# Kernel optimization log

Measured on AMD Instinct MI355X. Metric: run time of the kernel, lower is better.

## Reference

```python
import jax, jax.numpy as jnp
import numpy as np

B, N, C, H = 2, 2048, 1024, 16
D = C // H  # head_dim = 64


def setup_inputs() -> dict:
    key = jax.random.key(0)
    k1, k2, k3, k4 = jax.random.split(key, 4)
    x = jax.random.normal(k1, (B, N, C), dtype=jnp.float32)
    # params (torch Linear: y = x @ W.T + b). Store as [in, out] for einsum.
    w_qkv = jax.random.normal(k2, (C, 3 * C), dtype=jnp.float32) * (1.0 / np.sqrt(C))
    w_out = jax.random.normal(k3, (C, C), dtype=jnp.float32) * (1.0 / np.sqrt(C))
    b_out = jax.random.normal(k4, (C,), dtype=jnp.float32) * 0.01
    # causal mask: 1 above the diagonal -> masked_fill(-inf)
    attn_mask = jnp.triu(jnp.ones((N, N), dtype=jnp.int32), k=1)
    return {"x": x, "w_qkv": w_qkv, "w_out": w_out, "b_out": b_out, "attn_mask": attn_mask}


def reference(x, w_qkv, w_out, b_out, attn_mask):
    b, n, c = x.shape
    scale = 1.0 / jnp.sqrt(jnp.asarray(D, dtype=x.dtype))
    qkv = jnp.einsum('bnc,cd->bnd', x, w_qkv)                # [B, N, 3C]
    qkv = qkv.reshape(b, n, 3, H, D)
    q = qkv[:, :, 0].transpose(0, 2, 1, 3)                   # [B, H, N, D]
    k = qkv[:, :, 1].transpose(0, 2, 1, 3)
    v = qkv[:, :, 2].transpose(0, 2, 1, 3)
    scores = jnp.einsum('bhqd,bhkd->bhqk', q, k) * scale     # [B, H, N, N]
    scores = jnp.where(attn_mask == 1, jnp.asarray(-jnp.inf, dtype=scores.dtype), scores)
    attn = jax.nn.softmax(scores, axis=-1)
    # dropout is identity in eval mode (deterministic reference)
    out = jnp.einsum('bhqk,bhkd->bhqd', attn, v)             # [B, H, N, D]
    out = out.transpose(0, 2, 1, 3).reshape(b, n, c)         # [B, N, C]
    return jnp.einsum('bnc,cd->bnd', out, w_out) + b_out
```

## Files before the change

kernel.cpp:

```cpp
#include <hip/hip_runtime.h>

typedef _Float16 f16;
typedef _Float16 f16x8 __attribute__((ext_vector_type(8)));
typedef _Float16 f16x4 __attribute__((ext_vector_type(4)));
typedef float    f32x4 __attribute__((ext_vector_type(4)));

#define MFMA16(a, b, c) __builtin_amdgcn_mfma_f32_16x16x32_f16((a), (b), (c), 0, 0, 0)

__device__ __forceinline__ void gload16(const void* g, void* l) {
  __builtin_amdgcn_global_load_lds(
      (const __attribute__((address_space(1))) unsigned int*)g,
      (__attribute__((address_space(3))) unsigned int*)l, 16, 0, 0);
}

__device__ __forceinline__ float ex2(float x) {
  float r;
  asm("v_exp_f32 %0, %1" : "=v"(r) : "v"(x));
  return r;
}

#define WAITV(N) asm volatile("s_waitcnt vmcnt(" #N ")" ::: "memory")
#define BARRIER() __builtin_amdgcn_s_barrier()
#define CFENCE() asm volatile("" ::: "memory")

__global__ void prep(const float* __restrict__ x, f16* __restrict__ xh,
                     const float* __restrict__ wqkv, f16* __restrict__ oqkv,
                     const float* __restrict__ wout, f16* __restrict__ oout) {
  __shared__ float tile[32][33];
  int bx = blockIdx.x, t = threadIdx.x;
  if (bx < 4096) {
    int i = bx * 256 + t;
    float4 v = ((const float4*)x)[i];
    f16x4 o;
    o.x = (f16)v.x; o.y = (f16)v.y; o.z = (f16)v.z; o.w = (f16)v.w;
    ((f16x4*)xh)[i] = o;
    return;
  }
  int tb = bx - 4096;
  int bx2 = tb & 127, by = tb >> 7;
  const float* in;
  f16* out;
  int Cc, c0;
  if (bx2 < 96) { in = wqkv; out = oqkv; Cc = 3072; c0 = bx2 * 32; }
  else          { in = wout; out = oout; Cc = 1024; c0 = (bx2 - 96) * 32; }
  int r0 = by * 32;
  int tx = t & 31, ty = t >> 5;
#pragma unroll
  for (int i = ty; i < 32; i += 8)
    tile[i][tx] = in[(size_t)(r0 + i) * Cc + c0 + tx];
  __syncthreads();
#pragma unroll
  for (int i = ty; i < 32; i += 8)
    out[(size_t)(c0 + i) * 1024 + r0 + tx] = (f16)tile[tx][i];
}

template <int KDIM>
__device__ __forceinline__ void gemm_core(const f16* __restrict__ A, const f16* __restrict__ Bt,
                                          int bm, int bn, f16* lA, f16* lB, f32x4 acc[4][4]) {
  const int t = threadIdx.x, lane = t & 63, wave = t >> 6;
  const int wm = wave >> 1, wn = wave & 1;
  const int srow = lane >> 3;
  const int skb = (lane & 7) * 16;
  const int nkt = KDIM / 64;
  for (int kt = 0; kt < nkt; ++kt) {
    __syncthreads();
#pragma unroll
    for (int c = 0; c < 4; ++c) {
      int cc = c * 4 + wave;
      int row = cc * 8 + srow;
      int kbs = skb ^ ((row & 7) << 4);
      gload16((const char*)A + (size_t)(bm * 128 + row) * (KDIM * 2) + kt * 128 + kbs,
              lA + cc * 512);
      gload16((const char*)Bt + (size_t)(bn * 128 + row) * (KDIM * 2) + kt * 128 + kbs,
              lB + cc * 512);
    }
    __syncthreads();
#pragma unroll
    for (int ks = 0; ks < 2; ++ks) {
      f16x8 af[4], bf[4];
#pragma unroll
      for (int mi = 0; mi < 4; ++mi) {
        int r = wm * 64 + mi * 16 + (lane & 15);
        int ke = (ks * 32 + ((lane >> 4) << 3)) ^ ((r & 7) << 3);
        af[mi] = *(const f16x8*)&lA[r * 64 + ke];
      }
#pragma unroll
      for (int ni = 0; ni < 4; ++ni) {
        int r = wn * 64 + ni * 16 + (lane & 15);
        int ke = (ks * 32 + ((lane >> 4) << 3)) ^ ((r & 7) << 3);
        bf[ni] = *(const f16x8*)&lB[r * 64 + ke];
      }
#pragma unroll
      for (int mi = 0; mi < 4; ++mi)
#pragma unroll
        for (int ni = 0; ni < 4; ++ni)
          acc[mi][ni] = MFMA16(af[mi], bf[ni], acc[mi][ni]);
    }
  }
}

template <int KDIM>
__device__ __forceinline__ void gemm_core64(const f16* __restrict__ A, const f16* __restrict__ Bt,
                                            int bm, int bn, f16* lA, f16* lB, f32x4 acc[2][4]) {
  const int t = threadIdx.x, lane = t & 63, wave = t >> 6;
  const int wm = wave >> 1, wn = wave & 1;
  const int srow = lane >> 3;
  const int skb = (lane & 7) * 16;
  const int nkt = KDIM / 64;
  for (int kt = 0; kt < nkt; ++kt) {
    __syncthreads();
#pragma unroll
    for (int c = 0; c < 2; ++c) {
      int cc = c * 4 + wave;
      int row = cc * 8 + srow;
      int kbs = skb ^ ((row & 7) << 4);
      gload16((const char*)A + (size_t)(bm * 64 + row) * (KDIM * 2) + kt * 128 + kbs,
              lA + cc * 512);
    }
#pragma unroll
    for (int c = 0; c < 4; ++c) {
      int cc = c * 4 + wave;
      int row = cc * 8 + srow;
      int kbs = skb ^ ((row & 7) << 4);
      gload16((const char*)Bt + (size_t)(bn * 128 + row) * (KDIM * 2) + kt * 128 + kbs,
              lB + cc * 512);
    }
    __syncthreads();
#pragma unroll
    for (int ks = 0; ks < 2; ++ks) {
      f16x8 af[2], bf[4];
#pragma unroll
      for (int mi = 0; mi < 2; ++mi) {
        int r = wm * 32 + mi * 16 + (lane & 15);
        int ke = (ks * 32 + ((lane >> 4) << 3)) ^ ((r & 7) << 3);
        af[mi] = *(const f16x8*)&lA[r * 64 + ke];
      }
#pragma unroll
      for (int ni = 0; ni < 4; ++ni) {
        int r = wn * 64 + ni * 16 + (lane & 15);
        int ke = (ks * 32 + ((lane >> 4) << 3)) ^ ((r & 7) << 3);
        bf[ni] = *(const f16x8*)&lB[r * 64 + ke];
      }
#pragma unroll
      for (int mi = 0; mi < 2; ++mi)
#pragma unroll
        for (int ni = 0; ni < 4; ++ni)
          acc[mi][ni] = MFMA16(af[mi], bf[ni], acc[mi][ni]);
    }
  }
}

__global__ __launch_bounds__(256, 2) void gemm_qkv(const f16* __restrict__ A,
                                                   const f16* __restrict__ Bt,
                                                   f16* __restrict__ Qo, f16* __restrict__ Ko,
                                                   f16* __restrict__ Vt) {
  __shared__ __align__(16) f16 smem[128 * 136];
  f16* lA = smem;
  f16* lB = smem + 8192;
  f32x4 acc[4][4] = {};
  int w = blockIdx.x;
  int xcd = w & 7, i = w >> 3;
  int xr = xcd >> 1, xc = xcd & 1;
  int bm = xr * 8 + (i & 7);
  int bn = xc * 12 + (i >> 3);
  gemm_core<1024>(A, Bt, bm, bn, lA, lB, acc);
  int lane = threadIdx.x & 63, wave = threadIdx.x >> 6;
  int wm = wave >> 1, wn = wave & 1;
  int g = lane >> 4, q15 = lane & 15;
  int sec = (bn * 128) >> 10;
  if (sec < 2) {
    float scl = (sec == 0) ? 0.18033688f : 1.0f;
#pragma unroll
    for (int mi = 0; mi < 4; ++mi)
#pragma unroll
      for (int ni = 0; ni < 4; ++ni)
#pragma unroll
        for (int reg = 0; reg < 4; ++reg) {
          int gr = bm * 128 + wm * 64 + mi * 16 + (g << 2) + reg;
          int gc = bn * 128 + wn * 64 + ni * 16 + q15;
          int b = gr >> 11, n = gr & 2047;
          int jj = gc & 1023;
          int h = jj >> 6, d = jj & 63;
          f16 v = (f16)(acc[mi][ni][reg] * scl);
          size_t bh = (size_t)(b * 16 + h);
          if (sec == 0) Qo[(bh * 2048 + n) * 64 + d] = v;
          else          Ko[(bh * 2048 + n) * 64 + d] = v;
        }
  } else {
    __syncthreads();
#pragma unroll
    for (int mi = 0; mi < 4; ++mi)
#pragma unroll
      for (int ni = 0; ni < 4; ++ni)
#pragma unroll
        for (int reg = 0; reg < 4; ++reg) {
          int rl = wm * 64 + mi * 16 + (g << 2) + reg;
          int cl = wn * 64 + ni * 16 + q15;
          int r5 = rl & 31;
          int rlp = (rl & ~31) | (((r5 >> 2) & 3) << 3) | (((r5 >> 4) & 1) << 2) | (r5 & 3);
          smem[cl * 136 + rlp] = (f16)acc[mi][ni][reg];
        }
    __syncthreads();
    int tid = threadIdx.x;
    int cl = tid >> 1, half = tid & 1;
    int jj = (bn * 128 + cl) & 1023;
    int h = jj >> 6, d = jj & 63;
    int b = (bm * 128) >> 11;
    size_t bh = (size_t)(b * 16 + h);
    f16* dst = Vt + (bh * 64 + d) * 2048 + (bm * 128 & 2047) + half * 64;
    const f16* src = smem + cl * 136 + half * 64;
#pragma unroll
    for (int j8 = 0; j8 < 8; ++j8)
      *(f16x8*)&dst[j8 * 8] = *(const f16x8*)&src[j8 * 8];
  }
}

__device__ __forceinline__ void attn_one(const f16* __restrict__ Qb, const f16* __restrict__ Kb,
                                         const f16* __restrict__ Vb, f16* __restrict__ Ob,
                                         int qt, int lane, int wave, f16* lK, f16* lV) {
  const int N = 2048;
  const int wq0 = qt * 64 + wave * 16;
  const int g = lane >> 4, q15 = lane & 15;
  f16x8 qf[2];
#pragma unroll
  for (int ks = 0; ks < 2; ++ks)
    qf[ks] = *(const f16x8*)&Qb[(size_t)(wq0 + q15) * 64 + ks * 32 + (g << 3)];
  f32x4 oacc[4] = {};
  float mrun = -1e30f, lrun = 0.f;
  const int srow = lane >> 3, skb = (lane & 7) * 16;
  const int ntiles = qt + 1;

  auto STAGE = [&](int buf, int kv) {
    int kv0 = kv << 6;
#pragma unroll
    for (int c = 0; c < 2; ++c) {
      int cc = c * 4 + wave;
      int row = cc * 8 + srow;
      int kbs = skb ^ ((row & 7) << 4);
      gload16((const char*)Kb + (size_t)(kv0 + row) * 128 + kbs, lK + buf * 4096 + cc * 512);
      gload16((const char*)Vb + (size_t)row * (N * 2) + (size_t)kv0 * 2 + kbs,
              lV + buf * 4096 + cc * 512);
    }
  };

  STAGE(0, 0);
  if (ntiles > 1) STAGE(1, 1);
  for (int kv = 0; kv < ntiles; ++kv) {
    int cur = kv & 1;
    if (kv + 1 < ntiles) WAITV(4); else WAITV(0);
    BARRIER();
    const f16* K0 = lK + cur * 4096;
    const f16* V0 = lV + cur * 4096;
    int kv0 = kv << 6;
    f32x4 s[4] = {};
    __builtin_amdgcn_s_setprio(1);
#pragma unroll
    for (int ks = 0; ks < 2; ++ks) {
      f16x8 kf[4];
#pragma unroll
      for (int ni = 0; ni < 4; ++ni) {
        int r = ni * 16 + q15;
        int ke = (ks * 32 + (g << 3)) ^ ((r & 7) << 3);
        kf[ni] = *(const f16x8*)&K0[r * 64 + ke];
      }
#pragma unroll
      for (int ni = 0; ni < 4; ++ni) s[ni] = MFMA16(kf[ni], qf[ks], s[ni]);
    }
    __builtin_amdgcn_s_setprio(0);
    if (kv == qt) {
      int gq = wq0 + q15;
#pragma unroll
      for (int ni = 0; ni < 4; ++ni)
#pragma unroll
        for (int reg = 0; reg < 4; ++reg) {
          int gk = kv0 + ni * 16 + g * 4 + reg;
          if (gk > gq) s[ni][reg] = -1e30f;
        }
    }
    f32x4 m4 = s[0];
#pragma unroll
    for (int ni = 1; ni < 4; ++ni)
#pragma unroll
      for (int reg = 0; reg < 4; ++reg) m4[reg] = fmaxf(m4[reg], s[ni][reg]);
    float mx = fmaxf(fmaxf(m4[0], m4[1]), fmaxf(m4[2], m4[3]));
    mx = fmaxf(mx, __shfl_xor(mx, 16));
    mx = fmaxf(mx, __shfl_xor(mx, 32));
    if (__any(mx > mrun)) {
      float mnew = fmaxf(mrun, mx);
      float corr = ex2(mrun - mnew);
      mrun = mnew;
      lrun *= corr;
#pragma unroll
      for (int ni = 0; ni < 4; ++ni)
#pragma unroll
        for (int reg = 0; reg < 4; ++reg) oacc[ni][reg] *= corr;
    }
#pragma unroll
    for (int ni = 0; ni < 4; ++ni)
#pragma unroll
      for (int reg = 0; reg < 4; ++reg) s[ni][reg] = ex2(s[ni][reg] - mrun);
    f32x4 racc = (s[0] + s[1]) + (s[2] + s[3]);
    float rsum = (racc[0] + racc[1]) + (racc[2] + racc[3]);
    rsum += __shfl_xor(rsum, 16);
    rsum += __shfl_xor(rsum, 32);
    lrun += rsum;
    f16x8 pf[2];
#pragma unroll
    for (int ks = 0; ks < 2; ++ks)
#pragma unroll
      for (int e = 0; e < 8; ++e) pf[ks][e] = (f16)s[2 * ks + (e >> 2)][e & 3];
    __builtin_amdgcn_s_setprio(1);
#pragma unroll
    for (int ks = 0; ks < 2; ++ks) {
      f16x8 vf[4];
#pragma unroll
      for (int mi = 0; mi < 4; ++mi) {
        int r = mi * 16 + q15;
        int ke = (ks * 32 + (g << 3)) ^ ((r & 7) << 3);
        vf[mi] = *(const f16x8*)&V0[r * 64 + ke];
      }
#pragma unroll
      for (int mi = 0; mi < 4; ++mi) oacc[mi] = MFMA16(vf[mi], pf[ks], oacc[mi]);
    }
    __builtin_amdgcn_s_setprio(0);
    BARRIER();
    CFENCE();
    if (kv + 2 < ntiles) STAGE(cur, kv + 2);
  }
  float inv = 1.0f / lrun;
  int gq = wq0 + q15;
#pragma unroll
  for (int mi = 0; mi < 4; ++mi) {
    f16x4 o4;
#pragma unroll
    for (int reg = 0; reg < 4; ++reg) o4[reg] = (f16)(oacc[mi][reg] * inv);
    *(f16x4*)&Ob[(size_t)gq * 1024 + mi * 16 + g * 4] = o4;
  }
}

__global__ __launch_bounds__(256, 4) void attn(const f16* __restrict__ Q,
                                               const f16* __restrict__ K,
                                               const f16* __restrict__ Vt,
                                               f16* __restrict__ O) {
  __shared__ __align__(16) f16 lK[2 * 4096];
  __shared__ __align__(16) f16 lV[2 * 4096];
  int w = blockIdx.x;
  int c = w & 7, j = w >> 3;
  int a = j >> 5, k = j & 31;
  int bh = c * 4 + a;
  int kk = (a >= 2) ? ((k + 8) & 31) : k;
  int qt = (a & 1) ? (31 - kk) : kk;
  int b = bh >> 4, h = bh & 15;
  int lane = threadIdx.x & 63, wave = threadIdx.x >> 6;
  const f16* Qb = Q + (size_t)bh * 2048 * 64;
  const f16* Kb = K + (size_t)bh * 2048 * 64;
  const f16* Vb = Vt + (size_t)bh * 2048 * 64;
  f16* Ob = O + (size_t)b * 2048 * 1024 + h * 64;
  attn_one(Qb, Kb, Vb, Ob, qt, lane, wave, lK, lV);
}

__global__ __launch_bounds__(256, 2) void gemm_out(const f16* __restrict__ A,
                                                   const f16* __restrict__ Bt,
                                                   const float* __restrict__ bias,
                                                   float* __restrict__ out) {
  __shared__ __align__(16) f16 smem[12288];
  f16* lA = smem;
  f16* lB = smem + 4096;
  f32x4 acc[2][4] = {};
  int w = blockIdx.x;
  int xcd = w & 7, i = w >> 3;
  int bm = xcd * 8 + (i & 7);
  int bn = i >> 3;
  gemm_core64<1024>(A, Bt, bm, bn, lA, lB, acc);
  int lane = threadIdx.x & 63, wave = threadIdx.x >> 6;
  int wm = wave >> 1, wn = wave & 1;
#pragma unroll
  for (int mi = 0; mi < 2; ++mi)
#pragma unroll
    for (int ni = 0; ni < 4; ++ni)
#pragma unroll
      for (int reg = 0; reg < 4; ++reg) {
        int gr = bm * 64 + wm * 32 + mi * 16 + ((lane >> 4) << 2) + reg;
        int gc = bn * 128 + wn * 64 + ni * 16 + (lane & 15);
        out[(size_t)gr * 1024 + gc] = acc[mi][ni][reg] + bias[gc];
      }
}

extern "C" void kernel_launch(void* const* d_in, const int* in_sizes, int n_in,
                              void* d_out, int out_size, void* d_ws, size_t ws_size,
                              hipStream_t stream) {
  const float* x     = (const float*)d_in[0];
  const float* w_qkv = (const float*)d_in[1];
  const float* w_out = (const float*)d_in[2];
  const float* b_out = (const float*)d_in[3];
  float* out = (float*)d_out;
  char* ws = (char*)d_ws;

  f16* xh    = (f16*)(ws);
  f16* wqkvT = (f16*)(ws + (8u << 20));
  f16* woutT = (f16*)(ws + (14u << 20));
  f16* Qs    = (f16*)(ws + (16u << 20));
  f16* Ks    = (f16*)(ws + (24u << 20));
  f16* Vts   = (f16*)(ws + (32u << 20));
  f16* Oa    = (f16*)(ws + (40u << 20));

  prep<<<4096 + 128 * 32, 256, 0, stream>>>(x, xh, w_qkv, wqkvT, w_out, woutT);
  gemm_qkv<<<768, 256, 0, stream>>>(xh, wqkvT, Qs, Ks, Vts);
  attn<<<1024, 256, 0, stream>>>(Qs, Ks, Vts, Oa);
  gemm_out<<<512, 256, 0, stream>>>(Oa, woutT, b_out, out);
}
```

Baseline: 100.8 us.

## Split attention KV range across two wave pairs with 32-row KV tiles and merge

Restructures the attention kernel so the block's four waves form two pairs. Each pair processes half of the causal KV range in 32-key tiles, and each wave handles 32 query rows instead of 16. At the end, pair 1 writes its partial output, running max and running sum to LDS, and pair 0 merges them with a rescaling step. The intent is to halve the serial KV loop length per block and reuse each K/V fragment across two query subtiles, at the cost of a final merge step, extra LDS traffic and more registers.

```diff
diff --git a/kernel.cpp b/kernel.cpp
--- a/kernel.cpp
+++ b/kernel.cpp
@@ -215,135 +215,11 @@
   }
 }
 
-__device__ __forceinline__ void attn_one(const f16* __restrict__ Qb, const f16* __restrict__ Kb,
-                                         const f16* __restrict__ Vb, f16* __restrict__ Ob,
-                                         int qt, int lane, int wave, f16* lK, f16* lV) {
-  const int N = 2048;
-  const int wq0 = qt * 64 + wave * 16;
-  const int g = lane >> 4, q15 = lane & 15;
-  f16x8 qf[2];
-#pragma unroll
-  for (int ks = 0; ks < 2; ++ks)
-    qf[ks] = *(const f16x8*)&Qb[(size_t)(wq0 + q15) * 64 + ks * 32 + (g << 3)];
-  f32x4 oacc[4] = {};
-  float mrun = -1e30f, lrun = 0.f;
-  const int srow = lane >> 3, skb = (lane & 7) * 16;
-  const int ntiles = qt + 1;
-
-  auto STAGE = [&](int buf, int kv) {
-    int kv0 = kv << 6;
-#pragma unroll
-    for (int c = 0; c < 2; ++c) {
-      int cc = c * 4 + wave;
-      int row = cc * 8 + srow;
-      int kbs = skb ^ ((row & 7) << 4);
-      gload16((const char*)Kb + (size_t)(kv0 + row) * 128 + kbs, lK + buf * 4096 + cc * 512);
-      gload16((const char*)Vb + (size_t)row * (N * 2) + (size_t)kv0 * 2 + kbs,
-              lV + buf * 4096 + cc * 512);
-    }
-  };
-
-  STAGE(0, 0);
-  if (ntiles > 1) STAGE(1, 1);
-  for (int kv = 0; kv < ntiles; ++kv) {
-    int cur = kv & 1;
-    if (kv + 1 < ntiles) WAITV(4); else WAITV(0);
-    BARRIER();
-    const f16* K0 = lK + cur * 4096;
-    const f16* V0 = lV + cur * 4096;
-    int kv0 = kv << 6;
-    f32x4 s[4] = {};
-    __builtin_amdgcn_s_setprio(1);
-#pragma unroll
-    for (int ks = 0; ks < 2; ++ks) {
-      f16x8 kf[4];
-#pragma unroll
-      for (int ni = 0; ni < 4; ++ni) {
-        int r = ni * 16 + q15;
-        int ke = (ks * 32 + (g << 3)) ^ ((r & 7) << 3);
-        kf[ni] = *(const f16x8*)&K0[r * 64 + ke];
-      }
-#pragma unroll
-      for (int ni = 0; ni < 4; ++ni) s[ni] = MFMA16(kf[ni], qf[ks], s[ni]);
-    }
-    __builtin_amdgcn_s_setprio(0);
-    if (kv == qt) {
-      int gq = wq0 + q15;
-#pragma unroll
-      for (int ni = 0; ni < 4; ++ni)
-#pragma unroll
-        for (int reg = 0; reg < 4; ++reg) {
-          int gk = kv0 + ni * 16 + g * 4 + reg;
-          if (gk > gq) s[ni][reg] = -1e30f;
-        }
-    }
-    f32x4 m4 = s[0];
-#pragma unroll
-    for (int ni = 1; ni < 4; ++ni)
-#pragma unroll
-      for (int reg = 0; reg < 4; ++reg) m4[reg] = fmaxf(m4[reg], s[ni][reg]);
-    float mx = fmaxf(fmaxf(m4[0], m4[1]), fmaxf(m4[2], m4[3]));
-    mx = fmaxf(mx, __shfl_xor(mx, 16));
-    mx = fmaxf(mx, __shfl_xor(mx, 32));
-    if (__any(mx > mrun)) {
-      float mnew = fmaxf(mrun, mx);
-      float corr = ex2(mrun - mnew);
-      mrun = mnew;
-      lrun *= corr;
-#pragma unroll
-      for (int ni = 0; ni < 4; ++ni)
-#pragma unroll
-        for (int reg = 0; reg < 4; ++reg) oacc[ni][reg] *= corr;
-    }
-#pragma unroll
-    for (int ni = 0; ni < 4; ++ni)
-#pragma unroll
-      for (int reg = 0; reg < 4; ++reg) s[ni][reg] = ex2(s[ni][reg] - mrun);
-    f32x4 racc = (s[0] + s[1]) + (s[2] + s[3]);
-    float rsum = (racc[0] + racc[1]) + (racc[2] + racc[3]);
-    rsum += __shfl_xor(rsum, 16);
-    rsum += __shfl_xor(rsum, 32);
-    lrun += rsum;
-    f16x8 pf[2];
-#pragma unroll
-    for (int ks = 0; ks < 2; ++ks)
-#pragma unroll
-      for (int e = 0; e < 8; ++e) pf[ks][e] = (f16)s[2 * ks + (e >> 2)][e & 3];
-    __builtin_amdgcn_s_setprio(1);
-#pragma unroll
-    for (int ks = 0; ks < 2; ++ks) {
-      f16x8 vf[4];
-#pragma unroll
-      for (int mi = 0; mi < 4; ++mi) {
-        int r = mi * 16 + q15;
-        int ke = (ks * 32 + (g << 3)) ^ ((r & 7) << 3);
-        vf[mi] = *(const f16x8*)&V0[r * 64 + ke];
-      }
-#pragma unroll
-      for (int mi = 0; mi < 4; ++mi) oacc[mi] = MFMA16(vf[mi], pf[ks], oacc[mi]);
-    }
-    __builtin_amdgcn_s_setprio(0);
-    BARRIER();
-    CFENCE();
-    if (kv + 2 < ntiles) STAGE(cur, kv + 2);
-  }
-  float inv = 1.0f / lrun;
-  int gq = wq0 + q15;
-#pragma unroll
-  for (int mi = 0; mi < 4; ++mi) {
-    f16x4 o4;
-#pragma unroll
-    for (int reg = 0; reg < 4; ++reg) o4[reg] = (f16)(oacc[mi][reg] * inv);
-    *(f16x4*)&Ob[(size_t)gq * 1024 + mi * 16 + g * 4] = o4;
-  }
-}
-
 __global__ __launch_bounds__(256, 4) void attn(const f16* __restrict__ Q,
                                                const f16* __restrict__ K,
                                                const f16* __restrict__ Vt,
                                                f16* __restrict__ O) {
-  __shared__ __align__(16) f16 lK[2 * 4096];
-  __shared__ __align__(16) f16 lV[2 * 4096];
+  __shared__ __align__(16) f16 lds[16384];
   int w = blockIdx.x;
   int c = w & 7, j = w >> 3;
   int a = j >> 5, k = j & 31;
@@ -351,12 +227,174 @@
   int kk = (a >= 2) ? ((k + 8) & 31) : k;
   int qt = (a & 1) ? (31 - kk) : kk;
   int b = bh >> 4, h = bh & 15;
-  int lane = threadIdx.x & 63, wave = threadIdx.x >> 6;
+  const int t = threadIdx.x, lane = t & 63, wave = t >> 6;
+  const int pair = wave >> 1, rw = wave & 1;
+  const int g = lane >> 4, q15 = lane & 15;
   const f16* Qb = Q + (size_t)bh * 2048 * 64;
   const f16* Kb = K + (size_t)bh * 2048 * 64;
   const f16* Vb = Vt + (size_t)bh * 2048 * 64;
   f16* Ob = O + (size_t)b * 2048 * 1024 + h * 64;
-  attn_one(Qb, Kb, Vb, Ob, qt, lane, wave, lK, lV);
+  f16* lK = lds + pair * 4096;
+  f16* lV = lds + 8192 + pair * 4096;
+
+  const int base = qt * 64 + rw * 32;
+  f16x8 qf[2][2];
+#pragma unroll
+  for (int qm = 0; qm < 2; ++qm)
+#pragma unroll
+    for (int ks = 0; ks < 2; ++ks)
+      qf[qm][ks] = *(const f16x8*)&Qb[(size_t)(base + qm * 16 + q15) * 64 + ks * 32 + (g << 3)];
+  f32x4 oacc[2][4] = {};
+  float mrun[2] = {-1e30f, -1e30f}, lrun[2] = {0.f, 0.f};
+  const int nt = qt + 1;
+  const int kvoff = pair * nt;
+  const int ksrow = lane >> 3, kskb = (lane & 7) * 16;
+  const int vsrow = lane >> 2, vsg = lane & 3;
+
+  auto STAGE = [&](int buf, int i) {
+    int kv0 = (kvoff + i) << 5;
+#pragma unroll
+    for (int c2 = 0; c2 < 2; ++c2) {
+      int cc = c2 * 2 + rw;
+      {
+        int row = cc * 8 + ksrow;
+        int kbs = kskb ^ ((row & 7) << 4);
+        gload16((const char*)Kb + (size_t)(kv0 + row) * 128 + kbs, lK + buf * 2048 + cc * 512);
+      }
+      {
+        int row = cc * 16 + vsrow;
+        int gsw = vsg ^ (row & 3);
+        gload16((const char*)Vb + (size_t)row * 4096 + (size_t)kv0 * 2 + gsw * 16,
+                lV + buf * 2048 + cc * 512);
+      }
+    }
+  };
+
+  STAGE(0, 0);
+  if (nt > 1) STAGE(1, 1);
+  for (int i = 0; i < nt; ++i) {
+    int cur = i & 1;
+    if (i + 1 < nt) WAITV(4); else WAITV(0);
+    BARRIER();
+    const f16* K0 = lK + cur * 2048;
+    const f16* V0 = lV + cur * 2048;
+    int kvg = kvoff + i;
+    bool live = (kvg <= 2 * qt + rw);
+    if (live) {
+      f32x4 s[2][2] = {};
+      __builtin_amdgcn_s_setprio(1);
+#pragma unroll
+      for (int ks = 0; ks < 2; ++ks) {
+        f16x8 kf[2];
+#pragma unroll
+        for (int ni = 0; ni < 2; ++ni) {
+          int r = ni * 16 + q15;
+          int ke = (ks * 32 + (g << 3)) ^ ((r & 7) << 3);
+          kf[ni] = *(const f16x8*)&K0[r * 64 + ke];
+        }
+#pragma unroll
+        for (int qm = 0; qm < 2; ++qm)
+#pragma unroll
+          for (int ni = 0; ni < 2; ++ni)
+            s[qm][ni] = MFMA16(kf[ni], qf[qm][ks], s[qm][ni]);
+      }
+      __builtin_amdgcn_s_setprio(0);
+      if (kvg == 2 * qt + rw) {
+#pragma unroll
+        for (int qm = 0; qm < 2; ++qm) {
+          int gq = base + qm * 16 + q15;
+#pragma unroll
+          for (int ni = 0; ni < 2; ++ni)
+#pragma unroll
+            for (int reg = 0; reg < 4; ++reg) {
+              int gk = kvg * 32 + ni * 16 + g * 4 + reg;
+              if (gk > gq) s[qm][ni][reg] = -1e30f;
+            }
+        }
+      }
+      f16x8 pf[2];
+#pragma unroll
+      for (int qm = 0; qm < 2; ++qm) {
+        f32x4 m4 = s[qm][0];
+#pragma unroll
+        for (int reg = 0; reg < 4; ++reg) m4[reg] = fmaxf(m4[reg], s[qm][1][reg]);
+        float mx = fmaxf(fmaxf(m4[0], m4[1]), fmaxf(m4[2], m4[3]));
+        mx = fmaxf(mx, __shfl_xor(mx, 16));
+        mx = fmaxf(mx, __shfl_xor(mx, 32));
+        if (__any(mx > mrun[qm])) {
+          float mnew = fmaxf(mrun[qm], mx);
+          float corr = ex2(mrun[qm] - mnew);
+          mrun[qm] = mnew;
+          lrun[qm] *= corr;
+#pragma unroll
+          for (int dm = 0; dm < 4; ++dm)
+#pragma unroll
+            for (int reg = 0; reg < 4; ++reg) oacc[qm][dm][reg] *= corr;
+        }
+#pragma unroll
+        for (int ni = 0; ni < 2; ++ni)
+#pragma unroll
+          for (int reg = 0; reg < 4; ++reg) s[qm][ni][reg] = ex2(s[qm][ni][reg] - mrun[qm]);
+        f32x4 racc = s[qm][0] + s[qm][1];
+        float rsum = (racc[0] + racc[1]) + (racc[2] + racc[3]);
+        rsum += __shfl_xor(rsum, 16);
+        rsum += __shfl_xor(rsum, 32);
+        lrun[qm] += rsum;
+#pragma unroll
+        for (int e = 0; e < 8; ++e) pf[qm][e] = (f16)s[qm][e >> 2][e & 3];
+      }
+      __builtin_amdgcn_s_setprio(1);
+      f16x8 vf[4];
+#pragma unroll
+      for (int dm = 0; dm < 4; ++dm) {
+        int r = dm * 16 + q15;
+        vf[dm] = *(const f16x8*)&V0[r * 32 + ((g ^ (r & 3)) << 3)];
+      }
+#pragma unroll
+      for (int qm = 0; qm < 2; ++qm)
+#pragma unroll
+        for (int dm = 0; dm < 4; ++dm)
+          oacc[qm][dm] = MFMA16(vf[dm], pf[qm], oacc[qm][dm]);
+      __builtin_amdgcn_s_setprio(0);
+    }
+    BARRIER();
+    CFENCE();
+    if (i + 2 < nt) STAGE(cur, i + 2);
+  }
+
+  float* Om = (float*)lds;
+  float* ml = (float*)(lds + 8704);
+  if (pair == 1) {
+#pragma unroll
+    for (int qm = 0; qm < 2; ++qm) {
+      int r = rw * 32 + qm * 16 + q15;
+      if (g == 0) { ml[r * 2] = mrun[qm]; ml[r * 2 + 1] = lrun[qm]; }
+#pragma unroll
+      for (int dm = 0; dm < 4; ++dm)
+        *(f32x4*)&Om[r * 68 + dm * 16 + g * 4] = oacc[qm][dm];
+    }
+  }
+  BARRIER();
+  if (pair == 0) {
+#pragma unroll
+    for (int qm = 0; qm < 2; ++qm) {
+      int r = rw * 32 + qm * 16 + q15;
+      float mB = ml[r * 2], lB = ml[r * 2 + 1];
+      float m = fmaxf(mrun[qm], mB);
+      float cA = ex2(mrun[qm] - m), cB = ex2(mB - m);
+      float inv = 1.0f / (lrun[qm] * cA + lB * cB);
+      int gq = qt * 64 + r;
+#pragma unroll
+      for (int dm = 0; dm < 4; ++dm) {
+        f32x4 ob = *(const f32x4*)&Om[r * 68 + dm * 16 + g * 4];
+        f16x4 o4;
+#pragma unroll
+        for (int reg = 0; reg < 4; ++reg)
+          o4[reg] = (f16)((oacc[qm][dm][reg] * cA + ob[reg] * cB) * inv);
+        *(f16x4*)&Ob[(size_t)gq * 1024 + dm * 16 + g * 4] = o4;
+      }
+    }
+  }
 }
 
 __global__ __launch_bounds__(256, 2) void gemm_out(const f16* __restrict__ A,
```

Result: slower. 108.1 us (+7.3%).

## Enlarge QKV GEMM tiles to 256x256 with double-buffered async LDS loads

Applied to the files above, without the earlier changes.

Rewrites the QKV projection GEMM to use 256x256 output tiles per 512-thread block, down from 128x128 per 256-thread block. K-tiles are double-buffered in LDS with vmcnt waits and raised wave priority during the MFMA phase. The aim is more reuse per loaded tile and overlap of global loads with compute. In exchange, only 192 blocks are launched for 256 CUs, and LDS use and register pressure rise. The V transpose epilogue now runs in two passes.

```diff
diff --git a/kernel.cpp b/kernel.cpp
--- a/kernel.cpp
+++ b/kernel.cpp
@@ -55,51 +55,6 @@
 }
 
 template <int KDIM>
-__device__ __forceinline__ void gemm_core(const f16* __restrict__ A, const f16* __restrict__ Bt,
-                                          int bm, int bn, f16* lA, f16* lB, f32x4 acc[4][4]) {
-  const int t = threadIdx.x, lane = t & 63, wave = t >> 6;
-  const int wm = wave >> 1, wn = wave & 1;
-  const int srow = lane >> 3;
-  const int skb = (lane & 7) * 16;
-  const int nkt = KDIM / 64;
-  for (int kt = 0; kt < nkt; ++kt) {
-    __syncthreads();
-#pragma unroll
-    for (int c = 0; c < 4; ++c) {
-      int cc = c * 4 + wave;
-      int row = cc * 8 + srow;
-      int kbs = skb ^ ((row & 7) << 4);
-      gload16((const char*)A + (size_t)(bm * 128 + row) * (KDIM * 2) + kt * 128 + kbs,
-              lA + cc * 512);
-      gload16((const char*)Bt + (size_t)(bn * 128 + row) * (KDIM * 2) + kt * 128 + kbs,
-              lB + cc * 512);
-    }
-    __syncthreads();
-#pragma unroll
-    for (int ks = 0; ks < 2; ++ks) {
-      f16x8 af[4], bf[4];
-#pragma unroll
-      for (int mi = 0; mi < 4; ++mi) {
-        int r = wm * 64 + mi * 16 + (lane & 15);
-        int ke = (ks * 32 + ((lane >> 4) << 3)) ^ ((r & 7) << 3);
-        af[mi] = *(const f16x8*)&lA[r * 64 + ke];
-      }
-#pragma unroll
-      for (int ni = 0; ni < 4; ++ni) {
-        int r = wn * 64 + ni * 16 + (lane & 15);
-        int ke = (ks * 32 + ((lane >> 4) << 3)) ^ ((r & 7) << 3);
-        bf[ni] = *(const f16x8*)&lB[r * 64 + ke];
-      }
-#pragma unroll
-      for (int mi = 0; mi < 4; ++mi)
-#pragma unroll
-        for (int ni = 0; ni < 4; ++ni)
-          acc[mi][ni] = MFMA16(af[mi], bf[ni], acc[mi][ni]);
-    }
-  }
-}
-
-template <int KDIM>
 __device__ __forceinline__ void gemm_core64(const f16* __restrict__ A, const f16* __restrict__ Bt,
                                             int bm, int bn, f16* lA, f16* lB, f32x4 acc[2][4]) {
   const int t = threadIdx.x, lane = t & 63, wave = t >> 6;
@@ -150,34 +105,82 @@
   }
 }
 
-__global__ __launch_bounds__(256, 2) void gemm_qkv(const f16* __restrict__ A,
-                                                   const f16* __restrict__ Bt,
-                                                   f16* __restrict__ Qo, f16* __restrict__ Ko,
-                                                   f16* __restrict__ Vt) {
-  __shared__ __align__(16) f16 smem[128 * 136];
+__global__ __launch_bounds__(512) void gemm_qkv(const f16* __restrict__ A,
+                                                const f16* __restrict__ Bt,
+                                                f16* __restrict__ Qo, f16* __restrict__ Ko,
+                                                f16* __restrict__ Vt) {
+  __shared__ __align__(16) f16 smem[65536];
   f16* lA = smem;
-  f16* lB = smem + 8192;
-  f32x4 acc[4][4] = {};
+  f16* lB = smem + 32768;
+  f32x4 acc[8][4] = {};
   int w = blockIdx.x;
   int xcd = w & 7, i = w >> 3;
   int xr = xcd >> 1, xc = xcd & 1;
-  int bm = xr * 8 + (i & 7);
-  int bn = xc * 12 + (i >> 3);
-  gemm_core<1024>(A, Bt, bm, bn, lA, lB, acc);
-  int lane = threadIdx.x & 63, wave = threadIdx.x >> 6;
-  int wm = wave >> 1, wn = wave & 1;
-  int g = lane >> 4, q15 = lane & 15;
-  int sec = (bn * 128) >> 10;
+  int bm = xr * 4 + (i & 3);
+  int bn = xc * 6 + (i >> 2);
+  const int t = threadIdx.x, lane = t & 63, wave = t >> 6;
+  const int wm = wave >> 2, wn = wave & 3;
+  const int g = lane >> 4, q15 = lane & 15;
+  const int srow = lane >> 3, skb = (lane & 7) * 16;
+
+  auto STAGE = [&](int slot, int kt) {
+#pragma unroll
+    for (int c = 0; c < 4; ++c) {
+      int cc = c * 8 + wave;
+      int row = cc * 8 + srow;
+      int kbs = skb ^ ((row & 7) << 4);
+      gload16((const char*)A + (size_t)(bm * 256 + row) * 2048 + kt * 128 + kbs,
+              lA + slot * 16384 + cc * 512);
+      gload16((const char*)Bt + (size_t)(bn * 256 + row) * 2048 + kt * 128 + kbs,
+              lB + slot * 16384 + cc * 512);
+    }
+  };
+
+  STAGE(0, 0);
+  STAGE(1, 1);
+  for (int kt = 0; kt < 16; ++kt) {
+    int cur = kt & 1;
+    if (kt + 1 < 16) WAITV(8); else WAITV(0);
+    BARRIER();
+    const f16* A0 = lA + cur * 16384;
+    const f16* B0 = lB + cur * 16384;
+    __builtin_amdgcn_s_setprio(1);
+#pragma unroll
+    for (int ks = 0; ks < 2; ++ks) {
+      f16x8 bf[4];
+#pragma unroll
+      for (int ni = 0; ni < 4; ++ni) {
+        int r = wn * 64 + ni * 16 + q15;
+        int ke = (ks * 32 + (g << 3)) ^ ((r & 7) << 3);
+        bf[ni] = *(const f16x8*)&B0[r * 64 + ke];
+      }
+#pragma unroll
+      for (int mi = 0; mi < 8; ++mi) {
+        int r = wm * 128 + mi * 16 + q15;
+        int ke = (ks * 32 + (g << 3)) ^ ((r & 7) << 3);
+        f16x8 af = *(const f16x8*)&A0[r * 64 + ke];
+#pragma unroll
+        for (int ni = 0; ni < 4; ++ni)
+          acc[mi][ni] = MFMA16(af, bf[ni], acc[mi][ni]);
+      }
+    }
+    __builtin_amdgcn_s_setprio(0);
+    BARRIER();
+    CFENCE();
+    if (kt + 2 < 16) STAGE(cur, kt + 2);
+  }
+
+  int sec = bn >> 2;
   if (sec < 2) {
     float scl = (sec == 0) ? 0.18033688f : 1.0f;
 #pragma unroll
-    for (int mi = 0; mi < 4; ++mi)
+    for (int mi = 0; mi < 8; ++mi)
 #pragma unroll
       for (int ni = 0; ni < 4; ++ni)
 #pragma unroll
         for (int reg = 0; reg < 4; ++reg) {
-          int gr = bm * 128 + wm * 64 + mi * 16 + (g << 2) + reg;
-          int gc = bn * 128 + wn * 64 + ni * 16 + q15;
+          int gr = bm * 256 + wm * 128 + mi * 16 + (g << 2) + reg;
+          int gc = bn * 256 + wn * 64 + ni * 16 + q15;
           int b = gr >> 11, n = gr & 2047;
           int jj = gc & 1023;
           int h = jj >> 6, d = jj & 63;
@@ -187,31 +190,36 @@
           else          Ko[(bh * 2048 + n) * 64 + d] = v;
         }
   } else {
-    __syncthreads();
-#pragma unroll
-    for (int mi = 0; mi < 4; ++mi)
-#pragma unroll
-      for (int ni = 0; ni < 4; ++ni)
-#pragma unroll
-        for (int reg = 0; reg < 4; ++reg) {
-          int rl = wm * 64 + mi * 16 + (g << 2) + reg;
-          int cl = wn * 64 + ni * 16 + q15;
-          int r5 = rl & 31;
-          int rlp = (rl & ~31) | (((r5 >> 2) & 3) << 3) | (((r5 >> 4) & 1) << 2) | (r5 & 3);
-          smem[cl * 136 + rlp] = (f16)acc[mi][ni][reg];
-        }
-    __syncthreads();
-    int tid = threadIdx.x;
-    int cl = tid >> 1, half = tid & 1;
-    int jj = (bn * 128 + cl) & 1023;
+    int b = (bm * 256) >> 11;
+    int nbase = (bm * 256) & 2047;
+    int cl2 = t >> 1, half = t & 1;
+    int jj = (bn * 256 + cl2) & 1023;
     int h = jj >> 6, d = jj & 63;
-    int b = (bm * 128) >> 11;
     size_t bh = (size_t)(b * 16 + h);
-    f16* dst = Vt + (bh * 64 + d) * 2048 + (bm * 128 & 2047) + half * 64;
-    const f16* src = smem + cl * 136 + half * 64;
-#pragma unroll
-    for (int j8 = 0; j8 < 8; ++j8)
-      *(f16x8*)&dst[j8 * 8] = *(const f16x8*)&src[j8 * 8];
+#pragma unroll
+    for (int p = 0; p < 2; ++p) {
+      __syncthreads();
+      if (wm == p) {
+#pragma unroll
+        for (int mi = 0; mi < 8; ++mi)
+#pragma unroll
+          for (int ni = 0; ni < 4; ++ni)
+#pragma unroll
+            for (int reg = 0; reg < 4; ++reg) {
+              int rl = mi * 16 + (g << 2) + reg;
+              int cl = wn * 64 + ni * 16 + q15;
+              int r5 = rl & 31;
+              int rlp = (rl & ~31) | (((r5 >> 2) & 3) << 3) | (((r5 >> 4) & 1) << 2) | (r5 & 3);
+              smem[cl * 136 + rlp] = (f16)acc[mi][ni][reg];
+            }
+      }
+      __syncthreads();
+      f16* dst = Vt + (bh * 64 + d) * 2048 + nbase + p * 128 + half * 64;
+      const f16* src = smem + cl2 * 136 + half * 64;
+#pragma unroll
+      for (int j8 = 0; j8 < 8; ++j8)
+        *(f16x8*)&dst[j8 * 8] = *(const f16x8*)&src[j8 * 8];
+    }
   }
 }
 
@@ -405,7 +413,7 @@
   f16* Oa    = (f16*)(ws + (40u << 20));
 
   prep<<<4096 + 128 * 32, 256, 0, stream>>>(x, xh, w_qkv, wqkvT, w_out, woutT);
-  gemm_qkv<<<768, 256, 0, stream>>>(xh, wqkvT, Qs, Ks, Vts);
+  gemm_qkv<<<192, 512, 0, stream>>>(xh, wqkvT, Qs, Ks, Vts);
   attn<<<1024, 256, 0, stream>>>(Qs, Ks, Vts, Oa);
   gemm_out<<<512, 256, 0, stream>>>(Oa, woutT, b_out, out);
 }
```

Measured after the change: 106.1 us. 5.3% more time.
